# Kernel optimization log

Measured on AMD Instinct MI355X. Metric: run time of the kernel, lower is better.

The kernel has to match this reference:

```python
import jax, jax.numpy as jnp
import numpy as np

N = 100000
E = 1600000
IN_F, HID, OUT = 64, 128, 64


def setup_inputs() -> dict:
    key = jax.random.key(0)
    ks = jax.random.split(key, 16)
    glorot = lambda k, shp: jax.random.normal(k, shp, jnp.float32) * (2.0 / (shp[0] + shp[1])) ** 0.5
    return {
        "features": jax.random.normal(ks[0], (N, IN_F), jnp.float32),
        "W_neigh1": glorot(ks[1], (IN_F, HID)),
        "W_self1": glorot(ks[2], (IN_F, HID)),
        "b1": jnp.zeros((HID,), jnp.float32),
        "W_neigh2": glorot(ks[3], (HID, HID)),
        "W_self2": glorot(ks[4], (HID, HID)),
        "b2": jnp.zeros((HID,), jnp.float32),
        "Wm1": glorot(ks[5], (HID, HID)),
        "bm1": jnp.zeros((HID,), jnp.float32),
        "Wm2": glorot(ks[6], (HID, OUT)),
        "bm2": jnp.zeros((OUT,), jnp.float32),
        "src": jax.random.randint(ks[7], (E,), 0, N, jnp.int64),
        "dst": jax.random.randint(ks[8], (E,), 0, N, jnp.int64),
    }


def _sage_conv(x, src, dst, W_neigh, W_self, b):
    # mean aggregation of in-neighbor messages (DGL SAGEConv 'mean')
    msg = x[src]                                            # [E, d]
    agg = jax.ops.segment_sum(msg, dst, num_segments=N)     # [N, d]
    deg = jax.ops.segment_sum(jnp.ones((E,), x.dtype), dst, num_segments=N)
    h_neigh = agg / jnp.maximum(deg, 1.0)[:, None]
    return x @ W_self + h_neigh @ W_neigh + b


def reference(features, W_neigh1, W_self1, b1, W_neigh2, W_self2, b2,
              Wm1, bm1, Wm2, bm2, src, dst):
    x = jax.nn.relu(_sage_conv(features, src, dst, W_neigh1, W_self1, b1))
    x = jax.nn.relu(_sage_conv(x, src, dst, W_neigh2, W_self2, b2))
    x = jax.nn.relu(x @ Wm1 + bm1)
    return x @ Wm2 + bm2
```

## Files before the change

kernel.cpp:

```cpp
#include <hip/hip_runtime.h>
#include <hip/hip_fp8.h>

#define N_IN 64
#define HID 128
#define OUT_F 64
#define EPB 6144
#define BKT 128

typedef unsigned short ushort_t;
typedef unsigned char  uchar_t;
typedef ushort_t us8  __attribute__((ext_vector_type(8)));
typedef uchar_t  uc8  __attribute__((ext_vector_type(8)));
typedef short    s16x8 __attribute__((ext_vector_type(8)));
typedef float    f32x4 __attribute__((ext_vector_type(4)));
typedef float    f32x2 __attribute__((ext_vector_type(2)));
typedef unsigned int uint2v __attribute__((ext_vector_type(2)));

__device__ inline ushort_t f2bf(float f) {
    unsigned u = __float_as_uint(f);
    u = u + 0x7fffu + ((u >> 16) & 1u);
    return (ushort_t)(u >> 16);
}
__device__ inline float bf2f(ushort_t b) {
    return __uint_as_float((unsigned)b << 16);
}
__device__ inline uchar_t f2fp8(float v) {
    __hip_fp8_e4m3 q(v);
    return (uchar_t)q.__x;
}
template<bool HI>
__device__ inline f32x2 fp8pair(unsigned int dw) {
#if __has_builtin(__builtin_amdgcn_cvt_pk_f32_fp8)
    auto r = __builtin_amdgcn_cvt_pk_f32_fp8(dw, HI);
    f32x2 o; o[0] = r[0]; o[1] = r[1];
    return o;
#else
    f32x2 o;
#pragma unroll
    for (int i = 0; i < 2; ++i) {
        __hip_fp8_e4m3 h; h.__x = (dw >> (8 * (2 * (int)HI + i))) & 0xff;
        o[i] = (float)h;
    }
    return o;
#endif
}

__global__ __launch_bounds__(256)
void prep_kernel(const float* __restrict__ feat, ushort_t* __restrict__ featb,
                 uchar_t* __restrict__ featq, int n8,
                 const float* __restrict__ Ws1, const float* __restrict__ Wn1,
                 const float* __restrict__ Ws2, const float* __restrict__ Wn2,
                 const float* __restrict__ Wm1, const float* __restrict__ Wm2,
                 ushort_t* __restrict__ wsT1, ushort_t* __restrict__ wnT1,
                 ushort_t* __restrict__ wsT2, ushort_t* __restrict__ wnT2,
                 ushort_t* __restrict__ wmT1, ushort_t* __restrict__ wmT2,
                 const int* __restrict__ dst, int* __restrict__ histT,
                 int E, int nbuk, int nba, int BA, int BB) {
    __shared__ int hist[800];
    int b = blockIdx.x;
    int tid = threadIdx.x;
    if (b < BA) {
        int i = b * 256 + tid;
        if (i >= n8) return;
        f32x4 a = ((const f32x4*)feat)[2 * i];
        f32x4 c = ((const f32x4*)feat)[2 * i + 1];
        us8 v; uc8 q;
#pragma unroll
        for (int t = 0; t < 4; ++t) {
            v[t] = f2bf(a[t]); v[4 + t] = f2bf(c[t]);
            q[t] = f2fp8(a[t]); q[4 + t] = f2fp8(c[t]);
        }
        ((us8*)featb)[i] = v;
        ((uc8*)featq)[i] = q;
    } else if (b < BB) {
        int i = (b - BA) * 256 + tid;
        const float* W; ushort_t* WT; int K, H, l;
        if      (i < 8192)  { W = Ws1; WT = wsT1; K = 64;  H = 128; l = i; }
        else if (i < 16384) { W = Wn1; WT = wnT1; K = 64;  H = 128; l = i - 8192; }
        else if (i < 32768) { W = Ws2; WT = wsT2; K = 128; H = 128; l = i - 16384; }
        else if (i < 49152) { W = Wn2; WT = wnT2; K = 128; H = 128; l = i - 32768; }
        else if (i < 65536) { W = Wm1; WT = wmT1; K = 128; H = 128; l = i - 49152; }
        else if (i < 73728) { W = Wm2; WT = wmT2; K = 128; H = 64;  l = i - 65536; }
        else return;
        int h = l / K, k = l % K;
        WT[l] = f2bf(W[(size_t)k * H + h]);
    } else {
        const int blk  = b - BB;
        const int base = blk * EPB;
        for (int k = tid; k < nbuk; k += 256) hist[k] = 0;
        __syncthreads();
#pragma unroll
        for (int it = 0; it < EPB / 256; ++it) {
            int e = base + it * 256 + tid;
            if (e < E) atomicAdd(&hist[(unsigned)dst[e] / BKT], 1);
        }
        __syncthreads();
        for (int k = tid; k < nbuk; k += 256)
            histT[(size_t)k * nba + blk] = hist[k];
    }
}

__global__ __launch_bounds__(256)
void scan_block(const int* __restrict__ in, int* __restrict__ out,
                int* __restrict__ partials, int n) {
    __shared__ int sm[256];
    int i = blockIdx.x * 256 + threadIdx.x;
    int v = (i < n) ? in[i] : 0;
    sm[threadIdx.x] = v;
    __syncthreads();
    for (int d = 1; d < 256; d <<= 1) {
        int t = (threadIdx.x >= d) ? sm[threadIdx.x - d] : 0;
        __syncthreads();
        sm[threadIdx.x] += t;
        __syncthreads();
    }
    if (i < n) out[i] = sm[threadIdx.x] - v;
    if (threadIdx.x == 255) partials[blockIdx.x] = sm[255];
}

__global__ __launch_bounds__(1024)
void scan_partials(int* __restrict__ partials, int nparts) {
    __shared__ int sm[1024];
    int i = threadIdx.x;
    int v = (i < nparts) ? partials[i] : 0;
    sm[i] = v;
    __syncthreads();
    for (int d = 1; d < 1024; d <<= 1) {
        int t = (i >= d) ? sm[i - d] : 0;
        __syncthreads();
        sm[i] += t;
        __syncthreads();
    }
    if (i < nparts) partials[i] = sm[i] - v;
}

__global__ __launch_bounds__(256)
void scan_add(int* __restrict__ arr, const int* __restrict__ partials, int n) {
    int i = blockIdx.x * 256 + threadIdx.x;
    if (i < n) arr[i] += partials[i >> 8];
}

__global__ __launch_bounds__(256)
void part_edges(const int* __restrict__ src, const int* __restrict__ dst,
                const int* __restrict__ histT, unsigned* __restrict__ epk,
                int E, int nbuk, int nba) {
    __shared__ int cur[800];
    const int blk  = blockIdx.x;
    const int base = blk * EPB;
    const int tid  = threadIdx.x;
    for (int k = tid; k < nbuk; k += 256)
        cur[k] = histT[(size_t)k * nba + blk];
    __syncthreads();
#pragma unroll
    for (int it = 0; it < EPB / 256; ++it) {
        int e = base + it * 256 + tid;
        if (e < E) {
            unsigned d = (unsigned)dst[e], s = (unsigned)src[e];
            int pos = atomicAdd(&cur[d / BKT], 1);
            epk[pos] = ((d & (BKT - 1)) << 17) | s;
        }
    }
}

__global__ __launch_bounds__(256)
void build_bucket(const unsigned* __restrict__ epk, const int* __restrict__ histT,
                  int* __restrict__ offs, float* __restrict__ invd,
                  int* __restrict__ csr_src, int nn, int E, int nbuk, int nba) {
    __shared__ int sm[BKT];
    __shared__ int cur[BKT];
    const int b   = blockIdx.x;
    const int b0  = b * BKT;
    const int tid = threadIdx.x;
    const int ebase = histT[(size_t)b * nba];
    const int eend  = (b == nbuk - 1) ? E : histT[(size_t)(b + 1) * nba];

    if (tid < BKT) sm[tid] = 0;
    __syncthreads();
    for (int j = ebase + tid; j < eend; j += 256)
        atomicAdd(&sm[epk[j] >> 17], 1);
    __syncthreads();
    const int deg = (tid < BKT) ? sm[tid] : 0;
    for (int d = 1; d < BKT; d <<= 1) {
        int t = (tid >= d && tid < BKT) ? sm[tid - d] : 0;
        __syncthreads();
        if (tid < BKT) sm[tid] += t;
        __syncthreads();
    }
    if (tid < BKT) {
        const int excl = sm[tid] - deg;
        const int n = b0 + tid;
        if (n < nn) {
            offs[n] = ebase + excl;
            invd[n] = 1.0f / fmaxf((float)deg, 1.0f);
        }
        if (b == nbuk - 1 && tid == 0) offs[nn] = E;
        cur[tid] = ebase + excl;
    }
    __syncthreads();
    for (int j = ebase + tid; j < eend; j += 256) {
        unsigned p = epk[j];
        int pos = atomicAdd(&cur[p >> 17], 1);
        csr_src[pos] = (int)(p & 0x1FFFFu);
    }
}

template<int D>
__global__ __launch_bounds__(256)
void gather_fp8(const uchar_t* __restrict__ xq, const int* __restrict__ csr_src,
                const int* __restrict__ offs, const float* __restrict__ invd,
                ushort_t* __restrict__ aggb, int nn) {
    constexpr int C  = D / 8;
    constexpr int NE = 64 / C;
    const int n = (blockIdx.x * 256 + threadIdx.x) >> 6;
    if (n >= nn) return;
    const int lane = threadIdx.x & 63;
    const int c  = lane % C;
    const int eg = lane / C;
    const uchar_t* tab = xq + (size_t)c * 8;

    const int beg = offs[n], end = offs[n + 1];
    f32x2 acc[4];
#pragma unroll
    for (int t = 0; t < 4; ++t) acc[t] = (f32x2){0.f, 0.f};

    int j = beg + eg;
    for (; j + 3 * NE < end; j += 4 * NE) {
        int s0 = csr_src[j],          s1 = csr_src[j + NE];
        int s2 = csr_src[j + 2 * NE], s3 = csr_src[j + 3 * NE];
        uint2v q0 = *(const uint2v*)(tab + (size_t)s0 * D);
        uint2v q1 = *(const uint2v*)(tab + (size_t)s1 * D);
        uint2v q2 = *(const uint2v*)(tab + (size_t)s2 * D);
        uint2v q3 = *(const uint2v*)(tab + (size_t)s3 * D);
#pragma unroll
        for (int d = 0; d < 2; ++d) {
            f32x2 l01 = fp8pair<false>(q0[d]) + fp8pair<false>(q1[d]);
            f32x2 l23 = fp8pair<false>(q2[d]) + fp8pair<false>(q3[d]);
            acc[2 * d] += l01 + l23;
            f32x2 h01 = fp8pair<true>(q0[d]) + fp8pair<true>(q1[d]);
            f32x2 h23 = fp8pair<true>(q2[d]) + fp8pair<true>(q3[d]);
            acc[2 * d + 1] += h01 + h23;
        }
    }
    if (j + NE < end) {
        int s0 = csr_src[j], s1 = csr_src[j + NE];
        uint2v q0 = *(const uint2v*)(tab + (size_t)s0 * D);
        uint2v q1 = *(const uint2v*)(tab + (size_t)s1 * D);
#pragma unroll
        for (int d = 0; d < 2; ++d) {
            acc[2 * d]     += fp8pair<false>(q0[d]) + fp8pair<false>(q1[d]);
            acc[2 * d + 1] += fp8pair<true>(q0[d]) + fp8pair<true>(q1[d]);
        }
        j += 2 * NE;
    }
    if (j < end) {
        int s = csr_src[j];
        uint2v q = *(const uint2v*)(tab + (size_t)s * D);
#pragma unroll
        for (int d = 0; d < 2; ++d) {
            acc[2 * d]     += fp8pair<false>(q[d]);
            acc[2 * d + 1] += fp8pair<true>(q[d]);
        }
    }

#pragma unroll
    for (int m = C; m < 64; m <<= 1) {
#pragma unroll
        for (int t = 0; t < 4; ++t) {
            acc[t][0] += __shfl_xor(acc[t][0], m, 64);
            acc[t][1] += __shfl_xor(acc[t][1], m, 64);
        }
    }

    if (eg == 0) {
        float iv = invd[n];
        us8 ov;
#pragma unroll
        for (int t = 0; t < 4; ++t) {
            ov[2 * t]     = f2bf(acc[t][0] * iv);
            ov[2 * t + 1] = f2bf(acc[t][1] * iv);
        }
        *(us8*)(aggb + (size_t)n * D + c * 8) = ov;
    }
}

template<int K, int H, bool NEIGH, bool RELU, bool OBF, bool OFP8>
__global__ __launch_bounds__(256)
void mfma_layer(const ushort_t* __restrict__ xb, const ushort_t* __restrict__ gb,
                const ushort_t* __restrict__ wsT, const ushort_t* __restrict__ wnT,
                const float* __restrict__ bias, void* __restrict__ out,
                uchar_t* __restrict__ outq, int nn) {
    constexpr int CH   = K / 8;
    constexpr int KS   = K / 32;
    constexpr int WTPW = H / 64;
    constexpr int PF   = CH / 4;

    __shared__ us8 xs[64][CH];
    __shared__ us8 gs[NEIGH ? 64 : 1][NEIGH ? CH : 1];

    const int tid  = threadIdx.x;
    const int lane = tid & 63;
    const int w    = tid >> 6;
    const int lr   = lane & 15;
    const int lk   = lane >> 4;

    s16x8 bws[WTPW][KS];
    s16x8 bwn[NEIGH ? WTPW : 1][NEIGH ? KS : 1];
#pragma unroll
    for (int t = 0; t < WTPW; ++t) {
        const size_t hrow = (size_t)((w * WTPW + t) * 16 + lr) * K;
#pragma unroll
        for (int ks = 0; ks < KS; ++ks) {
            bws[t][ks] = *(const s16x8*)(wsT + hrow + ks * 32 + lk * 8);
            if constexpr (NEIGH)
                bwn[t][ks] = *(const s16x8*)(wnT + hrow + ks * 32 + lk * 8);
        }
    }
    float bv[WTPW];
#pragma unroll
    for (int t = 0; t < WTPW; ++t) bv[t] = bias[(w * WTPW + t) * 16 + lr];

    const int ntiles = (nn + 63) >> 6;
    us8 pfx[PF], pfg[NEIGH ? PF : 1];
    const us8 z8 = {0, 0, 0, 0, 0, 0, 0, 0};

    auto loadpf = [&](int T) {
        const int base = T * 64;
#pragma unroll
        for (int q = 0; q < PF; ++q) {
            int idx = tid + q * 256, r = idx / CH, c = idx % CH, n = base + r;
            pfx[q] = (n < nn) ? *(const us8*)(xb + (size_t)n * K + c * 8) : z8;
            if constexpr (NEIGH)
                pfg[q] = (n < nn) ? *(const us8*)(gb + (size_t)n * K + c * 8) : z8;
        }
    };

    int tile = blockIdx.x;
    if (tile >= ntiles) return;
    loadpf(tile);

    while (true) {
        __syncthreads();
#pragma unroll
        for (int q = 0; q < PF; ++q) {
            int idx = tid + q * 256, r = idx / CH, c = idx % CH;
            int cs = c ^ (r & 7);
            xs[r][cs] = pfx[q];
            if constexpr (NEIGH) gs[r][cs] = pfg[q];
        }
        __syncthreads();

        const int row0 = tile * 64;
        tile += gridDim.x;
        if (tile < ntiles) loadpf(tile);

        f32x4 acc[4][WTPW];
#pragma unroll
        for (int rg = 0; rg < 4; ++rg)
#pragma unroll
            for (int t = 0; t < WTPW; ++t) acc[rg][t] = {0.f, 0.f, 0.f, 0.f};

#pragma unroll
        for (int rg = 0; rg < 4; ++rg) {
            const int R = rg * 16 + lr;
#pragma unroll
            for (int ks = 0; ks < KS; ++ks) {
                const int cs = (ks * 4 + lk) ^ (R & 7);
                s16x8 ax = (s16x8)xs[R][cs];
                s16x8 ag;
                if constexpr (NEIGH) ag = (s16x8)gs[R][cs];
#pragma unroll
                for (int t = 0; t < WTPW; ++t) {
                    acc[rg][t] = __builtin_amdgcn_mfma_f32_16x16x32_bf16(ax, bws[t][ks], acc[rg][t], 0, 0, 0);
                    if constexpr (NEIGH)
                        acc[rg][t] = __builtin_amdgcn_mfma_f32_16x16x32_bf16(ag, bwn[t][ks], acc[rg][t], 0, 0, 0);
                }
            }
        }

#pragma unroll
        for (int rg = 0; rg < 4; ++rg) {
#pragma unroll
            for (int t = 0; t < WTPW; ++t) {
                const int h = (w * WTPW + t) * 16 + lr;
#pragma unroll
                for (int j = 0; j < 4; ++j) {
                    int n = row0 + rg * 16 + lk * 4 + j;
                    if (n < nn) {
                        float v = acc[rg][t][j] + bv[t];
                        if constexpr (RELU) v = fmaxf(v, 0.f);
                        if constexpr (OBF)
                            ((ushort_t*)out)[(size_t)n * H + h] = f2bf(v);
                        else
                            ((float*)out)[(size_t)n * H + h] = v;
                        if constexpr (OFP8)
                            outq[(size_t)n * H + h] = f2fp8(v);
                    }
                }
            }
        }

        if (tile >= ntiles) break;
    }
}

__global__ __launch_bounds__(256)
void mfma_tail(const ushort_t* __restrict__ xb, const ushort_t* __restrict__ gb,
               const ushort_t* __restrict__ wsT2, const ushort_t* __restrict__ wnT2,
               const ushort_t* __restrict__ wmT1, const ushort_t* __restrict__ wmT2,
               const float* __restrict__ b2, const float* __restrict__ bm1,
               const float* __restrict__ bm2, float* __restrict__ out, int nn) {
    constexpr int CH = 16, KS = 4, PF = 4;
    __shared__ us8 xs[64][CH];
    __shared__ us8 gs[64][CH];
    ushort_t* xs16 = (ushort_t*)xs;
    ushort_t* gs16 = (ushort_t*)gs;

    const int tid  = threadIdx.x;
    const int lane = tid & 63;
    const int w    = tid >> 6;
    const int lr   = lane & 15;
    const int lk   = lane >> 4;

    s16x8 bws2[2][KS], bwn2[2][KS], bwm1[2][KS], bwm2[KS];
#pragma unroll
    for (int t = 0; t < 2; ++t) {
        const size_t hrow = (size_t)((w * 2 + t) * 16 + lr) * HID;
#pragma unroll
        for (int ks = 0; ks < KS; ++ks) {
            bws2[t][ks] = *(const s16x8*)(wsT2 + hrow + ks * 32 + lk * 8);
            bwn2[t][ks] = *(const s16x8*)(wnT2 + hrow + ks * 32 + lk * 8);
            bwm1[t][ks] = *(const s16x8*)(wmT1 + hrow + ks * 32 + lk * 8);
        }
    }
    {
        const size_t hrow = (size_t)(w * 16 + lr) * HID;
#pragma unroll
        for (int ks = 0; ks < KS; ++ks)
            bwm2[ks] = *(const s16x8*)(wmT2 + hrow + ks * 32 + lk * 8);
    }
    float bv2[2]  = {b2[(w * 2) * 16 + lr],  b2[(w * 2 + 1) * 16 + lr]};
    float bvm1[2] = {bm1[(w * 2) * 16 + lr], bm1[(w * 2 + 1) * 16 + lr]};
    float bvm2    = bm2[w * 16 + lr];

    const int ntiles = (nn + 63) >> 6;
    us8 pfx[PF], pfg[PF];
    const us8 z8 = {0, 0, 0, 0, 0, 0, 0, 0};

    auto loadpf = [&](int T) {
        const int base = T * 64;
#pragma unroll
        for (int q = 0; q < PF; ++q) {
            int idx = tid + q * 256, r = idx / CH, c = idx % CH, n = base + r;
            pfx[q] = (n < nn) ? *(const us8*)(xb + (size_t)n * HID + c * 8) : z8;
            pfg[q] = (n < nn) ? *(const us8*)(gb + (size_t)n * HID + c * 8) : z8;
        }
    };

    auto st_bf = [&](ushort_t* base, int r, int h, float v) {
        int c8 = h >> 3, e = h & 7;
        int cs = c8 ^ (r & 7);
        base[r * 128 + cs * 8 + e] = f2bf(v);
    };

    int tile = blockIdx.x;
    if (tile >= ntiles) return;
    loadpf(tile);

    while (true) {
        __syncthreads();
#pragma unroll
        for (int q = 0; q < PF; ++q) {
            int idx = tid + q * 256, r = idx / CH, c = idx % CH;
            int cs = c ^ (r & 7);
            xs[r][cs] = pfx[q];
            gs[r][cs] = pfg[q];
        }
        __syncthreads();

        const int row0 = tile * 64;
        tile += gridDim.x;
        if (tile < ntiles) loadpf(tile);

        f32x4 a1[4][2];
#pragma unroll
        for (int rg = 0; rg < 4; ++rg)
#pragma unroll
            for (int t = 0; t < 2; ++t) a1[rg][t] = {0.f, 0.f, 0.f, 0.f};
#pragma unroll
        for (int rg = 0; rg < 4; ++rg) {
            const int R = rg * 16 + lr;
#pragma unroll
            for (int ks = 0; ks < KS; ++ks) {
                const int cs = (ks * 4 + lk) ^ (R & 7);
                s16x8 ax = (s16x8)xs[R][cs];
                s16x8 ag = (s16x8)gs[R][cs];
#pragma unroll
                for (int t = 0; t < 2; ++t) {
                    a1[rg][t] = __builtin_amdgcn_mfma_f32_16x16x32_bf16(ax, bws2[t][ks], a1[rg][t], 0, 0, 0);
                    a1[rg][t] = __builtin_amdgcn_mfma_f32_16x16x32_bf16(ag, bwn2[t][ks], a1[rg][t], 0, 0, 0);
                }
            }
        }
        __syncthreads();
#pragma unroll
        for (int rg = 0; rg < 4; ++rg)
#pragma unroll
            for (int t = 0; t < 2; ++t) {
                const int h = (w * 2 + t) * 16 + lr;
#pragma unroll
                for (int j = 0; j < 4; ++j) {
                    int r = rg * 16 + lk * 4 + j;
                    st_bf(gs16, r, h, fmaxf(a1[rg][t][j] + bv2[t], 0.f));
                }
            }
        __syncthreads();

        f32x4 a2[4][2];
#pragma unroll
        for (int rg = 0; rg < 4; ++rg)
#pragma unroll
            for (int t = 0; t < 2; ++t) a2[rg][t] = {0.f, 0.f, 0.f, 0.f};
#pragma unroll
        for (int rg = 0; rg < 4; ++rg) {
            const int R = rg * 16 + lr;
#pragma unroll
            for (int ks = 0; ks < KS; ++ks) {
                const int cs = (ks * 4 + lk) ^ (R & 7);
                s16x8 ax = (s16x8)gs[R][cs];
#pragma unroll
                for (int t = 0; t < 2; ++t)
                    a2[rg][t] = __builtin_amdgcn_mfma_f32_16x16x32_bf16(ax, bwm1[t][ks], a2[rg][t], 0, 0, 0);
            }
        }
        __syncthreads();
#pragma unroll
        for (int rg = 0; rg < 4; ++rg)
#pragma unroll
            for (int t = 0; t < 2; ++t) {
                const int h = (w * 2 + t) * 16 + lr;
#pragma unroll
                for (int j = 0; j < 4; ++j) {
                    int r = rg * 16 + lk * 4 + j;
                    st_bf(xs16, r, h, fmaxf(a2[rg][t][j] + bvm1[t], 0.f));
                }
            }
        __syncthreads();

        f32x4 a3[4];
#pragma unroll
        for (int rg = 0; rg < 4; ++rg) a3[rg] = {0.f, 0.f, 0.f, 0.f};
#pragma unroll
        for (int rg = 0; rg < 4; ++rg) {
            const int R = rg * 16 + lr;
#pragma unroll
            for (int ks = 0; ks < KS; ++ks) {
                const int cs = (ks * 4 + lk) ^ (R & 7);
                s16x8 ax = (s16x8)xs[R][cs];
                a3[rg] = __builtin_amdgcn_mfma_f32_16x16x32_bf16(ax, bwm2[ks], a3[rg], 0, 0, 0);
            }
        }
        const int h3 = w * 16 + lr;
#pragma unroll
        for (int rg = 0; rg < 4; ++rg)
#pragma unroll
            for (int j = 0; j < 4; ++j) {
                int n = row0 + rg * 16 + lk * 4 + j;
                if (n < nn) out[(size_t)n * OUT_F + h3] = a3[rg][j] + bvm2;
            }

        if (tile >= ntiles) break;
    }
}

extern "C" void kernel_launch(void* const* d_in, const int* in_sizes, int n_in,
                              void* d_out, int out_size, void* d_ws, size_t ws_size,
                              hipStream_t stream) {
    const float* feat = (const float*)d_in[0];
    const float* Wn1  = (const float*)d_in[1];
    const float* Ws1  = (const float*)d_in[2];
    const float* b1   = (const float*)d_in[3];
    const float* Wn2  = (const float*)d_in[4];
    const float* Ws2  = (const float*)d_in[5];
    const float* b2   = (const float*)d_in[6];
    const float* Wm1  = (const float*)d_in[7];
    const float* bm1  = (const float*)d_in[8];
    const float* Wm2  = (const float*)d_in[9];
    const float* bm2  = (const float*)d_in[10];
    const int*   src  = (const int*)d_in[11];
    const int*   dst  = (const int*)d_in[12];

    const int nn = in_sizes[0] / N_IN;
    const int E  = in_sizes[11];

    const int nbuk  = (nn + BKT - 1) / BKT;
    const int nba   = (E + EPB - 1) / EPB;
    const int nhist = nbuk * nba;

    char* p = (char*)d_ws;
    auto alloc = [&](size_t bytes) { void* q = p; p += (bytes + 63) & ~(size_t)63; return q; };
    int*      offs     = (int*)alloc((size_t)(nn + 1) * 4);
    int*      partials = (int*)alloc(1024 * 4);
    float*    invd     = (float*)alloc((size_t)nn * 4);
    int*      histT    = (int*)alloc((size_t)nhist * 4);
    unsigned* epk      = (unsigned*)alloc((size_t)E * 4);
    int*      csr_src  = (int*)alloc((size_t)E * 4);
    ushort_t* wsT1     = (ushort_t*)alloc((size_t)N_IN * HID * 2);
    ushort_t* wnT1     = (ushort_t*)alloc((size_t)N_IN * HID * 2);
    ushort_t* wsT2     = (ushort_t*)alloc((size_t)HID * HID * 2);
    ushort_t* wnT2     = (ushort_t*)alloc((size_t)HID * HID * 2);
    ushort_t* wmT1     = (ushort_t*)alloc((size_t)HID * HID * 2);
    ushort_t* wmT2     = (ushort_t*)alloc((size_t)HID * OUT_F * 2);
    ushort_t* featb    = (ushort_t*)alloc((size_t)nn * N_IN * 2);
    uchar_t*  x1q      = (uchar_t*)alloc((size_t)nn * HID);
    ushort_t* x1b      = (ushort_t*)alloc((size_t)nn * HID * 2);
    ushort_t* agg2b    = (ushort_t*)alloc((size_t)nn * HID * 2);
    ushort_t* agg1b    = (ushort_t*)d_out;
    uchar_t*  featq    = (uchar_t*)d_out + (size_t)nn * N_IN * 2;

    const int ntiles = (nn + 63) / 64;
    const int NB     = ntiles < 768 ? ntiles : 768;
    const int NBT    = ntiles < 512 ? ntiles : 512;
    const int n8     = nn * (N_IN / 8);
    const int BA     = (n8 + 255) / 256;
    const int BB     = BA + (73728 + 255) / 256;
    const int BC     = BB + nba;

    prep_kernel<<<BC, 256, 0, stream>>>(
        feat, featb, featq, n8,
        Ws1, Wn1, Ws2, Wn2, Wm1, Wm2,
        wsT1, wnT1, wsT2, wnT2, wmT1, wmT2,
        dst, histT, E, nbuk, nba, BA, BB);

    const int nparts = (nhist + 255) / 256;
    scan_block<<<nparts, 256, 0, stream>>>(histT, histT, partials, nhist);
    scan_partials<<<1, 1024, 0, stream>>>(partials, nparts);
    scan_add<<<nparts, 256, 0, stream>>>(histT, partials, nhist);

    part_edges<<<nba, 256, 0, stream>>>(src, dst, histT, epk, E, nbuk, nba);
    build_bucket<<<nbuk, 256, 0, stream>>>(epk, histT, offs, invd, csr_src, nn, E, nbuk, nba);

    gather_fp8<N_IN><<<(nn + 3) / 4, 256, 0, stream>>>(
        featq, csr_src, offs, invd, agg1b, nn);
    mfma_layer<N_IN, HID, true, true, true, true><<<NB, 256, 0, stream>>>(
        featb, agg1b, wsT1, wnT1, b1, x1b, x1q, nn);

    gather_fp8<HID><<<(nn + 3) / 4, 256, 0, stream>>>(
        x1q, csr_src, offs, invd, agg2b, nn);

    mfma_tail<<<NBT, 256, 0, stream>>>(
        x1b, agg2b, wsT2, wnT2, wmT1, wmT2, b2, bm1, bm2, (float*)d_out, nn);
}
```

Baseline: 200.6 us.

## Fold scan_add into consumers, double edges per block, prefetch gather indices

Removes the scan_add kernel launch by having part_edges and build_bucket add the scanned partial offsets when they read histT. Doubles EPB so fewer histogram/partition blocks and a smaller histT are produced, with partial unrolling. Software-pipelines the fp8 gather loop by loading the next group of csr_src indices before consuming the current feature loads. Trades one launch and a pass over histT for extra reads of partials, and larger per-block work may reduce parallelism.

```diff
diff --git a/kernel.cpp b/kernel.cpp
--- a/kernel.cpp
+++ b/kernel.cpp
@@ -4,7 +4,7 @@
 #define N_IN 64
 #define HID 128
 #define OUT_F 64
-#define EPB 6144
+#define EPB 12288
 #define BKT 128
 
 typedef unsigned short ushort_t;
@@ -89,7 +89,7 @@
         const int base = blk * EPB;
         for (int k = tid; k < nbuk; k += 256) hist[k] = 0;
         __syncthreads();
-#pragma unroll
+#pragma unroll 4
         for (int it = 0; it < EPB / 256; ++it) {
             int e = base + it * 256 + tid;
             if (e < E) atomicAdd(&hist[(unsigned)dst[e] / BKT], 1);
@@ -135,23 +135,19 @@
 }
 
 __global__ __launch_bounds__(256)
-void scan_add(int* __restrict__ arr, const int* __restrict__ partials, int n) {
-    int i = blockIdx.x * 256 + threadIdx.x;
-    if (i < n) arr[i] += partials[i >> 8];
-}
-
-__global__ __launch_bounds__(256)
 void part_edges(const int* __restrict__ src, const int* __restrict__ dst,
-                const int* __restrict__ histT, unsigned* __restrict__ epk,
-                int E, int nbuk, int nba) {
+                const int* __restrict__ histT, const int* __restrict__ partials,
+                unsigned* __restrict__ epk, int E, int nbuk, int nba) {
     __shared__ int cur[800];
     const int blk  = blockIdx.x;
     const int base = blk * EPB;
     const int tid  = threadIdx.x;
-    for (int k = tid; k < nbuk; k += 256)
-        cur[k] = histT[(size_t)k * nba + blk];
+    for (int k = tid; k < nbuk; k += 256) {
+        size_t idx = (size_t)k * nba + blk;
+        cur[k] = histT[idx] + partials[idx >> 8];
+    }
     __syncthreads();
-#pragma unroll
+#pragma unroll 4
     for (int it = 0; it < EPB / 256; ++it) {
         int e = base + it * 256 + tid;
         if (e < E) {
@@ -164,15 +160,22 @@
 
 __global__ __launch_bounds__(256)
 void build_bucket(const unsigned* __restrict__ epk, const int* __restrict__ histT,
-                  int* __restrict__ offs, float* __restrict__ invd,
-                  int* __restrict__ csr_src, int nn, int E, int nbuk, int nba) {
+                  const int* __restrict__ partials, int* __restrict__ offs,
+                  float* __restrict__ invd, int* __restrict__ csr_src,
+                  int nn, int E, int nbuk, int nba) {
     __shared__ int sm[BKT];
     __shared__ int cur[BKT];
     const int b   = blockIdx.x;
     const int b0  = b * BKT;
     const int tid = threadIdx.x;
-    const int ebase = histT[(size_t)b * nba];
-    const int eend  = (b == nbuk - 1) ? E : histT[(size_t)(b + 1) * nba];
+    size_t i0 = (size_t)b * nba;
+    const int ebase = histT[i0] + partials[i0 >> 8];
+    int eend;
+    if (b == nbuk - 1) eend = E;
+    else {
+        size_t i1 = (size_t)(b + 1) * nba;
+        eend = histT[i1] + partials[i1 >> 8];
+    }
 
     if (tid < BKT) sm[tid] = 0;
     __syncthreads();
@@ -224,13 +227,23 @@
     for (int t = 0; t < 4; ++t) acc[t] = (f32x2){0.f, 0.f};
 
     int j = beg + eg;
-    for (; j + 3 * NE < end; j += 4 * NE) {
-        int s0 = csr_src[j],          s1 = csr_src[j + NE];
-        int s2 = csr_src[j + 2 * NE], s3 = csr_src[j + 3 * NE];
-        uint2v q0 = *(const uint2v*)(tab + (size_t)s0 * D);
-        uint2v q1 = *(const uint2v*)(tab + (size_t)s1 * D);
-        uint2v q2 = *(const uint2v*)(tab + (size_t)s2 * D);
-        uint2v q3 = *(const uint2v*)(tab + (size_t)s3 * D);
+    int i0, i1, i2, i3;
+    bool have4 = (j + 3 * NE < end);
+    if (have4) {
+        i0 = csr_src[j];          i1 = csr_src[j + NE];
+        i2 = csr_src[j + 2 * NE]; i3 = csr_src[j + 3 * NE];
+    }
+    while (have4) {
+        uint2v q0 = *(const uint2v*)(tab + (size_t)i0 * D);
+        uint2v q1 = *(const uint2v*)(tab + (size_t)i1 * D);
+        uint2v q2 = *(const uint2v*)(tab + (size_t)i2 * D);
+        uint2v q3 = *(const uint2v*)(tab + (size_t)i3 * D);
+        j += 4 * NE;
+        bool next4 = (j + 3 * NE < end);
+        if (next4) {
+            i0 = csr_src[j];          i1 = csr_src[j + NE];
+            i2 = csr_src[j + 2 * NE]; i3 = csr_src[j + 3 * NE];
+        }
 #pragma unroll
         for (int d = 0; d < 2; ++d) {
             f32x2 l01 = fp8pair<false>(q0[d]) + fp8pair<false>(q1[d]);
@@ -240,6 +253,7 @@
             f32x2 h23 = fp8pair<true>(q2[d]) + fp8pair<true>(q3[d]);
             acc[2 * d + 1] += h01 + h23;
         }
+        have4 = next4;
     }
     if (j + NE < end) {
         int s0 = csr_src[j], s1 = csr_src[j + NE];
@@ -634,10 +648,9 @@
     const int nparts = (nhist + 255) / 256;
     scan_block<<<nparts, 256, 0, stream>>>(histT, histT, partials, nhist);
     scan_partials<<<1, 1024, 0, stream>>>(partials, nparts);
-    scan_add<<<nparts, 256, 0, stream>>>(histT, partials, nhist);
-
-    part_edges<<<nba, 256, 0, stream>>>(src, dst, histT, epk, E, nbuk, nba);
-    build_bucket<<<nbuk, 256, 0, stream>>>(epk, histT, offs, invd, csr_src, nn, E, nbuk, nba);
+
+    part_edges<<<nba, 256, 0, stream>>>(src, dst, histT, partials, epk, E, nbuk, nba);
+    build_bucket<<<nbuk, 256, 0, stream>>>(epk, histT, partials, offs, invd, csr_src, nn, E, nbuk, nba);
 
     gather_fp8<N_IN><<<(nn + 3) / 4, 256, 0, stream>>>(
         featq, csr_src, offs, invd, agg1b, nn);
```

Measured after the change: 209.4 us. +4.4%, slower.
